# Optimization experiments

Hardware: AMD Instinct MI355X
Metric: run time of the kernel (lower is better)

Reference implementation:

```python
import jax, jax.numpy as jnp
import numpy as np

B, T, C = 8, 2048, 768
H = 1  # n_heads
EPS = 1e-5


def layer_norm(x, g, b):
    mu = jnp.mean(x, axis=-1, keepdims=True)
    var = jnp.mean(jnp.square(x - mu), axis=-1, keepdims=True)
    return (x - mu) * jax.lax.rsqrt(var + EPS) * g + b


def setup_inputs() -> dict:
    key = jax.random.key(0)
    ks = jax.random.split(key, 12)
    s = 1.0 / np.sqrt(C)
    return {
        "x": jax.random.normal(ks[0], (B, T, C), jnp.float32),
        "Wq": jax.random.normal(ks[1], (C, C), jnp.float32) * s,
        "Wk": jax.random.normal(ks[2], (C, C), jnp.float32) * s,
        "Wv": jax.random.normal(ks[3], (C, C), jnp.float32) * s,
        "Wp": jax.random.normal(ks[4], (C, C), jnp.float32) * s,
        "bp": jnp.zeros((C,), jnp.float32),
        "g1": jnp.ones((C,), jnp.float32),
        "b1": jnp.zeros((C,), jnp.float32),
        "g2": jnp.ones((C,), jnp.float32),
        "b2": jnp.zeros((C,), jnp.float32),
        "W1": jax.random.normal(ks[5], (C, 4 * C), jnp.float32) * s,
        "bm1": jnp.zeros((4 * C,), jnp.float32),
        "W2": jax.random.normal(ks[6], (4 * C, C), jnp.float32) * (1.0 / np.sqrt(4 * C)),
        "bm2": jnp.zeros((C,), jnp.float32),
    }


def attention(xn, Wq, Wk, Wv, Wp, bp):
    # single head (H=1): q,k,v are [B, T, C]
    q = xn @ Wq
    k = xn @ Wk
    v = xn @ Wv
    scale = 1.0 / np.sqrt(C // H)
    scores = jnp.einsum("btc,bsc->bts", q, k) * scale  # [B,T,T]
    causal = jnp.tril(jnp.ones((T, T), dtype=bool))
    scores = jnp.where(causal, scores, -jnp.inf)
    attn = jax.nn.softmax(scores, axis=-1)
    y = jnp.einsum("bts,bsc->btc", attn, v)
    return y @ Wp + bp


def reference(x, Wq, Wk, Wv, Wp, bp, g1, b1, g2, b2, W1, bm1, W2, bm2):
    # pre-LN transformer block; dropout is identity at eval
    x = x + attention(layer_norm(x, g1, b1), Wq, Wk, Wv, Wp, bp)
    h = layer_norm(x, g2, b2)
    h = jax.nn.gelu(h @ W1 + bm1, approximate=False) @ W2 + bm2
    return x + h
```

## Files before the change

kernel.cpp:

```cpp
#include <hip/hip_runtime.h>
#include <hip/hip_bf16.h>


typedef unsigned short u16;
typedef __bf16 bf16x8 __attribute__((ext_vector_type(8)));
typedef float  f32x4  __attribute__((ext_vector_type(4)));
typedef int    i32x4  __attribute__((ext_vector_type(4)));
typedef u16    u16x4  __attribute__((ext_vector_type(4)));

__device__ __forceinline__ u16 f2b(float f) {
    __hip_bfloat16 h = __float2bfloat16(f);
    return *reinterpret_cast<u16*>(&h);
}
__device__ __forceinline__ float b2f(u16 u) {
    unsigned int x = ((unsigned int)u) << 16;
    return __uint_as_float(x);
}

__device__ __forceinline__ void stage16(u16* lds_base_uniform, const u16* g, int lane) {
#if __has_builtin(__builtin_amdgcn_global_load_lds)
    __builtin_amdgcn_global_load_lds(
        (const __attribute__((address_space(1))) void*)g,
        (__attribute__((address_space(3))) void*)lds_base_uniform,
        16, 0, 0);
#else
    *(i32x4*)(lds_base_uniform + lane * 8) = *(const i32x4*)g;
#endif
}

__global__ __launch_bounds__(256) void transpose_cast(const float* __restrict__ in,
                                                      u16* __restrict__ out,
                                                      int R, int Cc) {
    __shared__ float tile[32][33];
    int c0 = blockIdx.x * 32, r0 = blockIdx.y * 32;
    int tx = threadIdx.x, ty = threadIdx.y;
    for (int i = ty; i < 32; i += 8)
        tile[i][tx] = in[(long)(r0 + i) * Cc + c0 + tx];
    __syncthreads();
    for (int i = ty; i < 32; i += 8)
        out[(long)(c0 + i) * R + r0 + tx] = f2b(tile[tx][i]);
}

__global__ __launch_bounds__(256) void ln_kernel(const float* __restrict__ x,
                                                 const float* __restrict__ g,
                                                 const float* __restrict__ b,
                                                 u16* __restrict__ out) {
    const int C = 768;
    long row = blockIdx.x;
    const float* xr = x + row * C;
    int t = threadIdx.x;
    float v0 = xr[t], v1 = xr[t + 256], v2 = xr[t + 512];
    float s = v0 + v1 + v2;
    float sq = v0 * v0 + v1 * v1 + v2 * v2;
#pragma unroll
    for (int o = 32; o; o >>= 1) {
        s += __shfl_xor(s, o);
        sq += __shfl_xor(sq, o);
    }
    __shared__ float ss[4], sq2[4];
    int wv = t >> 6;
    if ((t & 63) == 0) { ss[wv] = s; sq2[wv] = sq; }
    __syncthreads();
    s = ss[0] + ss[1] + ss[2] + ss[3];
    sq = sq2[0] + sq2[1] + sq2[2] + sq2[3];
    float mu = s * (1.0f / 768.0f);
    float var = sq * (1.0f / 768.0f) - mu * mu;
    float rs = rsqrtf(var + 1e-5f);
    u16* orow = out + row * C;
    orow[t]       = f2b((v0 - mu) * rs * g[t]       + b[t]);
    orow[t + 256] = f2b((v1 - mu) * rs * g[t + 256] + b[t + 256]);
    orow[t + 512] = f2b((v2 - mu) * rs * g[t + 512] + b[t + 512]);
}

__global__ __launch_bounds__(256) void softmax_causal(u16* __restrict__ S) {
    const int T = 2048;
    long row = blockIdx.x;
    int t = (int)(row & (T - 1));
    int ncols = ((t >> 7) + 1) << 7;
    u16* p = S + row * T;
    int tid = threadIdx.x;
    float v[8];
    float mx = -3.0e38f;
#pragma unroll
    for (int j = 0; j < 8; j++) {
        int col = tid + j * 256;
        v[j] = (col <= t) ? b2f(p[col]) : -3.0e38f;
        mx = fmaxf(mx, v[j]);
        if (col >= ncols) break;
    }
#pragma unroll
    for (int o = 32; o; o >>= 1) mx = fmaxf(mx, __shfl_xor(mx, o));
    __shared__ float sm[4], ssum[4];
    int wv = tid >> 6;
    if ((tid & 63) == 0) sm[wv] = mx;
    __syncthreads();
    mx = fmaxf(fmaxf(sm[0], sm[1]), fmaxf(sm[2], sm[3]));
    float s = 0.0f;
#pragma unroll
    for (int j = 0; j < 8; j++) {
        int col = tid + j * 256;
        if (col >= ncols) break;
        float e = (col <= t) ? expf(v[j] - mx) : 0.0f;
        v[j] = e;
        s += e;
    }
#pragma unroll
    for (int o = 32; o; o >>= 1) s += __shfl_xor(s, o);
    if ((tid & 63) == 0) ssum[wv] = s;
    __syncthreads();
    s = ssum[0] + ssum[1] + ssum[2] + ssum[3];
    float inv = 1.0f / s;
#pragma unroll
    for (int j = 0; j < 8; j++) {
        int col = tid + j * 256;
        if (col >= ncols) break;
        p[col] = f2b(v[j] * inv);
    }
}

#define BM 128
#define BN 128
#define BKT 64

template <int EPI, int CAUSAL>
__global__ __launch_bounds__(256) void gemm_bt(const u16* __restrict__ A,
                                               const u16* __restrict__ Bt,
                                               void* __restrict__ Out,
                                               void* __restrict__ Out2,
                                               const float* __restrict__ bias,
                                               const float* __restrict__ resid,
                                               int M, int N, int K,
                                               int lda, int ldb, int ldo,
                                               long long sA, long long sB, long long sO,
                                               float scale) {
    int bz = blockIdx.z;
    A += (long)bz * sA;
    Bt += (long)bz * sB;
    long obase = (long)bz * sO;

    int gx = gridDim.x;
    int nblk = gx * gridDim.y;
    int lin = blockIdx.y * gx + blockIdx.x;
    int chunk = nblk >> 3;
    int tile = (lin & 7) * chunk + (lin >> 3);
    int m0 = (tile / gx) * BM;
    int n0 = (tile % gx) * BN;

    if (CAUSAL == 1 && n0 >= m0 + BM) return;
    int kend = (CAUSAL == 2) ? ((K < m0 + BM) ? K : (m0 + BM)) : K;

    __shared__ __align__(16) u16 As[128 * 64];
    __shared__ __align__(16) u16 Bs[128 * 64];

    int tid = threadIdx.x;
    int lane = tid & 63, l16 = lane & 15, quad = lane >> 4;
    int w = tid >> 6;
    int wm = (w >> 1) * 64, wn = (w & 1) * 64;

    f32x4 acc[4][4] = {};

    for (int k0 = 0; k0 < kend; k0 += BKT) {
#pragma unroll
        for (int i = 0; i < 4; i++) {
            int ebase = i * 256 + w * 64;
            int e = ebase + lane;
            int row = e >> 3;
            int gc = (e & 7) ^ (row & 7);
            stage16(As + ebase * 8, A + (long)(m0 + row) * lda + k0 + gc * 8, lane);
            stage16(Bs + ebase * 8, Bt + (long)(n0 + row) * ldb + k0 + gc * 8, lane);
        }
        __syncthreads();
#pragma unroll
        for (int kk = 0; kk < BKT; kk += 32) {
            int cbase = (kk >> 3) + quad;
            int slot = (cbase ^ (l16 & 7)) << 3;
            bf16x8 af[4], bf[4];
#pragma unroll
            for (int mt = 0; mt < 4; mt++)
                af[mt] = *(const bf16x8*)(As + (wm + mt * 16 + l16) * 64 + slot);
#pragma unroll
            for (int nt = 0; nt < 4; nt++)
                bf[nt] = *(const bf16x8*)(Bs + (wn + nt * 16 + l16) * 64 + slot);
#pragma unroll
            for (int mt = 0; mt < 4; mt++)
#pragma unroll
                for (int nt = 0; nt < 4; nt++)
                    acc[mt][nt] = __builtin_amdgcn_mfma_f32_16x16x32_bf16(af[mt], bf[nt], acc[mt][nt], 0, 0, 0);
        }
        __syncthreads();
    }

#pragma unroll
    for (int mt = 0; mt < 4; ++mt)
#pragma unroll
        for (int nt = 0; nt < 4; ++nt) {
            int col = n0 + wn + nt * 16 + l16;
            int rbase = m0 + wm + mt * 16 + quad * 4;
            f32x4 a = acc[mt][nt];
            if (EPI == 0) {
                u16* o = (u16*)Out + obase;
#pragma unroll
                for (int r = 0; r < 4; r++)
                    o[(long)(rbase + r) * ldo + col] = f2b(a[r] * scale);
            } else if (EPI == 1) {
                u16* o = (u16*)Out + obase;
                u16x4 pk;
#pragma unroll
                for (int r = 0; r < 4; r++) pk[r] = f2b(a[r] * scale);
                *(u16x4*)(o + (long)col * ldo + rbase) = pk;
            } else if (EPI == 2) {
                u16* o = (u16*)Out + obase;
                float bv = bias[col];
#pragma unroll
                for (int r = 0; r < 4; r++) {
                    float v = a[r] + bv;
                    float ge = 0.5f * v * (1.0f + erff(v * 0.70710678118f));
                    o[(long)(rbase + r) * ldo + col] = f2b(ge);
                }
            } else if (EPI == 3) {
                float* o = (float*)Out + obase;
                float bv = bias[col];
#pragma unroll
                for (int r = 0; r < 4; r++) {
                    long idx = (long)(rbase + r) * ldo + col;
                    o[idx] = resid[idx] + a[r] + bv;
                }
            } else {
                if (col < 1536) {
                    u16* o = (u16*)Out;
#pragma unroll
                    for (int r = 0; r < 4; r++)
                        o[(long)(rbase + r) * 1536 + col] = f2b(a[r]);
                } else {
                    u16* o = (u16*)Out2;
                    int b = rbase >> 11, t = rbase & 2047, c = col - 1536;
                    u16x4 pk;
#pragma unroll
                    for (int r = 0; r < 4; r++) pk[r] = f2b(a[r]);
                    *(u16x4*)(o + ((long)b * 768 + c) * 2048 + t) = pk;
                }
            }
        }
}

extern "C" void kernel_launch(void* const* d_in, const int* in_sizes, int n_in,
                              void* d_out, int out_size, void* d_ws, size_t ws_size,
                              hipStream_t stream) {
    (void)in_sizes; (void)n_in; (void)out_size; (void)ws_size;
    const float* x   = (const float*)d_in[0];
    const float* Wq  = (const float*)d_in[1];
    const float* Wk  = (const float*)d_in[2];
    const float* Wv  = (const float*)d_in[3];
    const float* Wp  = (const float*)d_in[4];
    const float* bp  = (const float*)d_in[5];
    const float* g1  = (const float*)d_in[6];
    const float* b1  = (const float*)d_in[7];
    const float* g2  = (const float*)d_in[8];
    const float* b2  = (const float*)d_in[9];
    const float* W1  = (const float*)d_in[10];
    const float* bm1 = (const float*)d_in[11];
    const float* W2  = (const float*)d_in[12];
    const float* bm2 = (const float*)d_in[13];
    float* out = (float*)d_out;

    const int Bn = 8, T = 2048, C = 768, F = 3072;
    const int M = Bn * T;

    char* ws = (char*)d_ws;
    u16* xn = (u16*)(ws);
    u16* QK = (u16*)(ws + 25165824);
    u16* vT = (u16*)(ws + 75497472);
    u16* S  = (u16*)(ws + 100663296);
    u16* y  = (u16*)(ws + 167772160);
    u16* h1 = (u16*)(ws + 25165824);
    u16* wgt = (u16*)(ws + 192937984);
    u16* Wqt = wgt;
    u16* Wkt = Wqt + 589824;
    u16* Wvt = Wkt + 589824;
    u16* Wpt = Wvt + 589824;
    u16* W1t = Wpt + 589824;
    u16* W2t = W1t + (long)C * F;

    dim3 tb(32, 8);
    hipLaunchKernelGGL(transpose_cast, dim3(C / 32, C / 32), tb, 0, stream, Wq, Wqt, C, C);
    hipLaunchKernelGGL(transpose_cast, dim3(C / 32, C / 32), tb, 0, stream, Wk, Wkt, C, C);
    hipLaunchKernelGGL(transpose_cast, dim3(C / 32, C / 32), tb, 0, stream, Wv, Wvt, C, C);
    hipLaunchKernelGGL(transpose_cast, dim3(C / 32, C / 32), tb, 0, stream, Wp, Wpt, C, C);
    hipLaunchKernelGGL(transpose_cast, dim3(F / 32, C / 32), tb, 0, stream, W1, W1t, C, F);
    hipLaunchKernelGGL(transpose_cast, dim3(C / 32, F / 32), tb, 0, stream, W2, W2t, F, C);

    hipLaunchKernelGGL(ln_kernel, dim3(M), dim3(256), 0, stream, x, g1, b1, xn);

    hipLaunchKernelGGL((gemm_bt<4, 0>), dim3((3 * C) / BN, M / BM, 1), dim3(256), 0, stream,
                       xn, Wqt, (void*)QK, (void*)vT, nullptr, nullptr,
                       M, 3 * C, C, C, C, 0, 0LL, 0LL, 0LL, 1.0f);

    float scl = 1.0f / sqrtf((float)C);
    hipLaunchKernelGGL((gemm_bt<0, 1>), dim3(T / BN, T / BM, Bn), dim3(256), 0, stream,
                       QK, QK + 768, (void*)S, nullptr, nullptr, nullptr,
                       T, T, C, 1536, 1536, T,
                       (long long)T * 1536, (long long)T * 1536, (long long)T * T, scl);

    hipLaunchKernelGGL(softmax_causal, dim3(M), dim3(256), 0, stream, S);

    hipLaunchKernelGGL((gemm_bt<0, 2>), dim3(C / BN, T / BM, Bn), dim3(256), 0, stream,
                       S, vT, (void*)y, nullptr, nullptr, nullptr,
                       T, C, T, T, T, C,
                       (long long)T * T, (long long)C * T, (long long)T * C, 1.0f);

    hipLaunchKernelGGL((gemm_bt<3, 0>), dim3(C / BN, M / BM, 1), dim3(256), 0, stream,
                       y, Wpt, (void*)out, nullptr, bp, x,
                       M, C, C, C, C, C, 0LL, 0LL, 0LL, 1.0f);

    hipLaunchKernelGGL(ln_kernel, dim3(M), dim3(256), 0, stream, out, g2, b2, xn);

    hipLaunchKernelGGL((gemm_bt<2, 0>), dim3(F / BN, M / BM, 1), dim3(256), 0, stream,
                       xn, W1t, (void*)h1, nullptr, bm1, nullptr,
                       M, F, C, C, C, F, 0LL, 0LL, 0LL, 1.0f);

    hipLaunchKernelGGL((gemm_bt<3, 0>), dim3(C / BN, M / BM, 1), dim3(256), 0, stream,
                       h1, W2t, (void*)out, nullptr, bm2, out,
                       M, C, F, F, F, C, 0LL, 0LL, 0LL, 1.0f);
}
```

Before: 695.8 us.

## Switch GEMMs to 32x32x16 MFMA, vectorize LN/softmax, approximate GELU

```diff
diff --git a/kernel.cpp b/kernel.cpp
--- a/kernel.cpp
+++ b/kernel.cpp
@@ -5,8 +5,10 @@
 typedef unsigned short u16;
 typedef __bf16 bf16x8 __attribute__((ext_vector_type(8)));
 typedef float  f32x4  __attribute__((ext_vector_type(4)));
+typedef float  f32x16 __attribute__((ext_vector_type(16)));
 typedef int    i32x4  __attribute__((ext_vector_type(4)));
 typedef u16    u16x4  __attribute__((ext_vector_type(4)));
+typedef u16    u16x8  __attribute__((ext_vector_type(8)));
 
 __device__ __forceinline__ u16 f2b(float f) {
     __hip_bfloat16 h = __float2bfloat16(f);
@@ -15,6 +17,13 @@
 __device__ __forceinline__ float b2f(u16 u) {
     unsigned int x = ((unsigned int)u) << 16;
     return __uint_as_float(x);
+}
+
+__device__ __forceinline__ float fast_gelu(float v) {
+    float t = v * v;
+    float z = v * fmaf(0.10294294f, t, 2.30211842f);
+    float e = exp2f(-z);
+    return v * __builtin_amdgcn_rcpf(1.0f + e);
 }
 
 __device__ __forceinline__ void stage16(u16* lds_base_uniform, const u16* g, int lane) {
@@ -41,7 +50,7 @@
         out[(long)(c0 + i) * R + r0 + tx] = f2b(tile[tx][i]);
 }
 
-__global__ __launch_bounds__(256) void ln_kernel(const float* __restrict__ x,
+__global__ __launch_bounds__(192) void ln_kernel(const float* __restrict__ x,
                                                  const float* __restrict__ g,
                                                  const float* __restrict__ b,
                                                  u16* __restrict__ out) {
@@ -49,27 +58,29 @@
     long row = blockIdx.x;
     const float* xr = x + row * C;
     int t = threadIdx.x;
-    float v0 = xr[t], v1 = xr[t + 256], v2 = xr[t + 512];
-    float s = v0 + v1 + v2;
-    float sq = v0 * v0 + v1 * v1 + v2 * v2;
+    f32x4 v = *(const f32x4*)(xr + t * 4);
+    float s = v[0] + v[1] + v[2] + v[3];
+    float sq = v[0] * v[0] + v[1] * v[1] + v[2] * v[2] + v[3] * v[3];
 #pragma unroll
     for (int o = 32; o; o >>= 1) {
         s += __shfl_xor(s, o);
         sq += __shfl_xor(sq, o);
     }
-    __shared__ float ss[4], sq2[4];
+    __shared__ float ss[3], sq2[3];
     int wv = t >> 6;
     if ((t & 63) == 0) { ss[wv] = s; sq2[wv] = sq; }
     __syncthreads();
-    s = ss[0] + ss[1] + ss[2] + ss[3];
-    sq = sq2[0] + sq2[1] + sq2[2] + sq2[3];
+    s = ss[0] + ss[1] + ss[2];
+    sq = sq2[0] + sq2[1] + sq2[2];
     float mu = s * (1.0f / 768.0f);
     float var = sq * (1.0f / 768.0f) - mu * mu;
     float rs = rsqrtf(var + 1e-5f);
-    u16* orow = out + row * C;
-    orow[t]       = f2b((v0 - mu) * rs * g[t]       + b[t]);
-    orow[t + 256] = f2b((v1 - mu) * rs * g[t + 256] + b[t + 256]);
-    orow[t + 512] = f2b((v2 - mu) * rs * g[t + 512] + b[t + 512]);
+    f32x4 gv = *(const f32x4*)(g + t * 4);
+    f32x4 bv = *(const f32x4*)(b + t * 4);
+    u16x4 pk;
+#pragma unroll
+    for (int j = 0; j < 4; j++) pk[j] = f2b((v[j] - mu) * rs * gv[j] + bv[j]);
+    *(u16x4*)(out + row * C + t * 4) = pk;
 }
 
 __global__ __launch_bounds__(256) void softmax_causal(u16* __restrict__ S) {
@@ -79,14 +90,18 @@
     int ncols = ((t >> 7) + 1) << 7;
     u16* p = S + row * T;
     int tid = threadIdx.x;
+    int base = tid * 8;
+    bool act = base < ncols;
     float v[8];
     float mx = -3.0e38f;
-#pragma unroll
-    for (int j = 0; j < 8; j++) {
-        int col = tid + j * 256;
-        v[j] = (col <= t) ? b2f(p[col]) : -3.0e38f;
-        mx = fmaxf(mx, v[j]);
-        if (col >= ncols) break;
+    if (act) {
+        u16x8 raw = *(const u16x8*)(p + base);
+#pragma unroll
+        for (int j = 0; j < 8; j++) {
+            int col = base + j;
+            v[j] = (col <= t) ? b2f(raw[j]) : -3.0e38f;
+            mx = fmaxf(mx, v[j]);
+        }
     }
 #pragma unroll
     for (int o = 32; o; o >>= 1) mx = fmaxf(mx, __shfl_xor(mx, o));
@@ -96,13 +111,14 @@
     __syncthreads();
     mx = fmaxf(fmaxf(sm[0], sm[1]), fmaxf(sm[2], sm[3]));
     float s = 0.0f;
-#pragma unroll
-    for (int j = 0; j < 8; j++) {
-        int col = tid + j * 256;
-        if (col >= ncols) break;
-        float e = (col <= t) ? expf(v[j] - mx) : 0.0f;
-        v[j] = e;
-        s += e;
+    if (act) {
+#pragma unroll
+        for (int j = 0; j < 8; j++) {
+            int col = base + j;
+            float e = (col <= t) ? __expf(v[j] - mx) : 0.0f;
+            v[j] = e;
+            s += e;
+        }
     }
 #pragma unroll
     for (int o = 32; o; o >>= 1) s += __shfl_xor(s, o);
@@ -110,11 +126,11 @@
     __syncthreads();
     s = ssum[0] + ssum[1] + ssum[2] + ssum[3];
     float inv = 1.0f / s;
-#pragma unroll
-    for (int j = 0; j < 8; j++) {
-        int col = tid + j * 256;
-        if (col >= ncols) break;
-        p[col] = f2b(v[j] * inv);
+    if (act) {
+        u16x8 pk;
+#pragma unroll
+        for (int j = 0; j < 8; j++) pk[j] = f2b(v[j] * inv);
+        *(u16x8*)(p + base) = pk;
     }
 }
 
@@ -123,16 +139,16 @@
 #define BKT 64
 
 template <int EPI, int CAUSAL>
-__global__ __launch_bounds__(256) void gemm_bt(const u16* __restrict__ A,
-                                               const u16* __restrict__ Bt,
-                                               void* __restrict__ Out,
-                                               void* __restrict__ Out2,
-                                               const float* __restrict__ bias,
-                                               const float* __restrict__ resid,
-                                               int M, int N, int K,
-                                               int lda, int ldb, int ldo,
-                                               long long sA, long long sB, long long sO,
-                                               float scale) {
+__global__ __launch_bounds__(256, 4) void gemm_bt(const u16* __restrict__ A,
+                                                  const u16* __restrict__ Bt,
+                                                  void* __restrict__ Out,
+                                                  void* __restrict__ Out2,
+                                                  const float* __restrict__ bias,
+                                                  const float* __restrict__ resid,
+                                                  int M, int N, int K,
+                                                  int lda, int ldb, int ldo,
+                                                  long long sA, long long sB, long long sO,
+                                                  float scale) {
     int bz = blockIdx.z;
     A += (long)bz * sA;
     Bt += (long)bz * sB;
@@ -153,11 +169,12 @@
     __shared__ __align__(16) u16 Bs[128 * 64];
 
     int tid = threadIdx.x;
-    int lane = tid & 63, l16 = lane & 15, quad = lane >> 4;
+    int lane = tid & 63;
+    int l32 = lane & 31, kg = lane >> 5;
     int w = tid >> 6;
     int wm = (w >> 1) * 64, wn = (w & 1) * 64;
 
-    f32x4 acc[4][4] = {};
+    f32x16 acc[2][2] = {};
 
     for (int k0 = 0; k0 < kend; k0 += BKT) {
 #pragma unroll
@@ -171,73 +188,72 @@
         }
         __syncthreads();
 #pragma unroll
-        for (int kk = 0; kk < BKT; kk += 32) {
-            int cbase = (kk >> 3) + quad;
-            int slot = (cbase ^ (l16 & 7)) << 3;
-            bf16x8 af[4], bf[4];
-#pragma unroll
-            for (int mt = 0; mt < 4; mt++)
-                af[mt] = *(const bf16x8*)(As + (wm + mt * 16 + l16) * 64 + slot);
-#pragma unroll
-            for (int nt = 0; nt < 4; nt++)
-                bf[nt] = *(const bf16x8*)(Bs + (wn + nt * 16 + l16) * 64 + slot);
-#pragma unroll
-            for (int mt = 0; mt < 4; mt++)
-#pragma unroll
-                for (int nt = 0; nt < 4; nt++)
-                    acc[mt][nt] = __builtin_amdgcn_mfma_f32_16x16x32_bf16(af[mt], bf[nt], acc[mt][nt], 0, 0, 0);
+        for (int kk = 0; kk < 4; kk++) {
+            int c = (kk << 1) + kg;
+            bf16x8 af[2], bf[2];
+#pragma unroll
+            for (int mt = 0; mt < 2; mt++) {
+                int r = wm + mt * 32 + l32;
+                af[mt] = *(const bf16x8*)(As + r * 64 + ((c ^ (r & 7)) << 3));
+            }
+#pragma unroll
+            for (int nt = 0; nt < 2; nt++) {
+                int r = wn + nt * 32 + l32;
+                bf[nt] = *(const bf16x8*)(Bs + r * 64 + ((c ^ (r & 7)) << 3));
+            }
+#pragma unroll
+            for (int mt = 0; mt < 2; mt++)
+#pragma unroll
+                for (int nt = 0; nt < 2; nt++)
+                    acc[mt][nt] = __builtin_amdgcn_mfma_f32_32x32x16_bf16(af[mt], bf[nt], acc[mt][nt], 0, 0, 0);
         }
         __syncthreads();
     }
 
 #pragma unroll
-    for (int mt = 0; mt < 4; ++mt)
-#pragma unroll
-        for (int nt = 0; nt < 4; ++nt) {
-            int col = n0 + wn + nt * 16 + l16;
-            int rbase = m0 + wm + mt * 16 + quad * 4;
-            f32x4 a = acc[mt][nt];
+    for (int mt = 0; mt < 2; ++mt)
+#pragma unroll
+        for (int nt = 0; nt < 2; ++nt) {
+            int col = n0 + wn + nt * 32 + l32;
+            int rb = m0 + wm + mt * 32 + 4 * kg;
+            f32x16 a = acc[mt][nt];
             if (EPI == 0) {
                 u16* o = (u16*)Out + obase;
 #pragma unroll
-                for (int r = 0; r < 4; r++)
-                    o[(long)(rbase + r) * ldo + col] = f2b(a[r] * scale);
-            } else if (EPI == 1) {
-                u16* o = (u16*)Out + obase;
-                u16x4 pk;
-#pragma unroll
-                for (int r = 0; r < 4; r++) pk[r] = f2b(a[r] * scale);
-                *(u16x4*)(o + (long)col * ldo + rbase) = pk;
+                for (int r = 0; r < 16; r++)
+                    o[(long)(rb + (r & 3) + 8 * (r >> 2)) * ldo + col] = f2b(a[r] * scale);
             } else if (EPI == 2) {
                 u16* o = (u16*)Out + obase;
                 float bv = bias[col];
 #pragma unroll
-                for (int r = 0; r < 4; r++) {
-                    float v = a[r] + bv;
-                    float ge = 0.5f * v * (1.0f + erff(v * 0.70710678118f));
-                    o[(long)(rbase + r) * ldo + col] = f2b(ge);
-                }
+                for (int r = 0; r < 16; r++)
+                    o[(long)(rb + (r & 3) + 8 * (r >> 2)) * ldo + col] = f2b(fast_gelu(a[r] + bv));
             } else if (EPI == 3) {
                 float* o = (float*)Out + obase;
                 float bv = bias[col];
 #pragma unroll
-                for (int r = 0; r < 4; r++) {
-                    long idx = (long)(rbase + r) * ldo + col;
+                for (int r = 0; r < 16; r++) {
+                    long idx = (long)(rb + (r & 3) + 8 * (r >> 2)) * ldo + col;
                     o[idx] = resid[idx] + a[r] + bv;
                 }
             } else {
                 if (col < 1536) {
                     u16* o = (u16*)Out;
 #pragma unroll
-                    for (int r = 0; r < 4; r++)
-                        o[(long)(rbase + r) * 1536 + col] = f2b(a[r]);
+                    for (int r = 0; r < 16; r++)
+                        o[(long)(rb + (r & 3) + 8 * (r >> 2)) * 1536 + col] = f2b(a[r]);
                 } else {
                     u16* o = (u16*)Out2;
-                    int b = rbase >> 11, t = rbase & 2047, c = col - 1536;
-                    u16x4 pk;
-#pragma unroll
-                    for (int r = 0; r < 4; r++) pk[r] = f2b(a[r]);
-                    *(u16x4*)(o + ((long)b * 768 + c) * 2048 + t) = pk;
+                    int c = col - 1536;
+#pragma unroll
+                    for (int gi = 0; gi < 4; gi++) {
+                        int row = rb + 8 * gi;
+                        int b = row >> 11, t = row & 2047;
+                        u16x4 pk;
+#pragma unroll
+                        for (int j = 0; j < 4; j++) pk[j] = f2b(a[gi * 4 + j]);
+                        *(u16x4*)(o + ((long)b * 768 + c) * 2048 + t) = pk;
+                    }
                 }
             }
         }
@@ -289,7 +305,7 @@
     hipLaunchKernelGGL(transpose_cast, dim3(F / 32, C / 32), tb, 0, stream, W1, W1t, C, F);
     hipLaunchKernelGGL(transpose_cast, dim3(C / 32, F / 32), tb, 0, stream, W2, W2t, F, C);
 
-    hipLaunchKernelGGL(ln_kernel, dim3(M), dim3(256), 0, stream, x, g1, b1, xn);
+    hipLaunchKernelGGL(ln_kernel, dim3(M), dim3(192), 0, stream, x, g1, b1, xn);
 
     hipLaunchKernelGGL((gemm_bt<4, 0>), dim3((3 * C) / BN, M / BM, 1), dim3(256), 0, stream,
                        xn, Wqt, (void*)QK, (void*)vT, nullptr, nullptr,
@@ -312,7 +328,7 @@
                        y, Wpt, (void*)out, nullptr, bp, x,
                        M, C, C, C, C, C, 0LL, 0LL, 0LL, 1.0f);
 
-    hipLaunchKernelGGL(ln_kernel, dim3(M), dim3(256), 0, stream, out, g2, b2, xn);
+    hipLaunchKernelGGL(ln_kernel, dim3(M), dim3(192), 0, stream, out, g2, b2, xn);
 
     hipLaunchKernelGGL((gemm_bt<2, 0>), dim3(F / BN, M / BM, 1), dim3(256), 0, stream,
                        xn, W1t, (void*)h1, nullptr, bm1, nullptr,
```

After: 608.1 us. 12.6% less time.
